# Performance work log

Measured on AMD Instinct MI355X. Metric: run time of the kernel, lower is better.

## Reference

```python
import jax, jax.numpy as jnp
import numpy as np

SEQ, B, IN, H = 512, 256, 300, 256

def setup_inputs() -> dict:
    key = jax.random.key(0)
    ks = jax.random.split(key, 14)
    s = lambda *sh: 1.0 / np.sqrt(sh[0])
    inp = {
        'secuencia': jax.random.normal(ks[0], (SEQ, B, IN), jnp.float32),
        # RNN cell 1 (forward direction)
        'W1x': jax.random.normal(ks[1], (IN, H), jnp.float32) * s(IN),
        'W1h': jax.random.normal(ks[2], (H, H), jnp.float32) * s(H),
        'b1':  jax.random.normal(ks[3], (H,), jnp.float32) * 0.01,
        # RNN cell 2 (backward direction)
        'W2x': jax.random.normal(ks[4], (IN, H), jnp.float32) * s(IN),
        'W2h': jax.random.normal(ks[5], (H, H), jnp.float32) * s(H),
        'b2':  jax.random.normal(ks[6], (H,), jnp.float32) * 0.01,
        # MLP head (weights stored [in, out])
        'fc1_w': jax.random.normal(ks[7], (2 * H, 2 * H), jnp.float32) * s(2 * H),
        'fc1_b': jnp.zeros((2 * H,), jnp.float32),
        'fc2_w': jax.random.normal(ks[8], (2 * H, H), jnp.float32) * s(2 * H),
        'fc2_b': jnp.zeros((H,), jnp.float32),
        'fs_w':  jax.random.normal(ks[9], (H, 1), jnp.float32) * s(H),
        'fs_b':  jnp.zeros((1,), jnp.float32),
    }
    return inp

def _rnn_scan(seq, Wx, Wh, b):
    # seq: [S, B, IN] -> final hidden [B, H]; Elman cell h' = tanh(x Wx + h Wh + b)
    h0 = jnp.zeros((seq.shape[1], Wh.shape[0]), seq.dtype)
    def step(h, x):
        return jnp.tanh(x @ Wx + h @ Wh + b), None
    h_final, _ = jax.lax.scan(step, h0, seq)
    return h_final

def reference(secuencia, W1x, W1h, b1, W2x, W2h, b2,
              fc1_w, fc1_b, fc2_w, fc2_b, fs_w, fs_b):
    h1 = _rnn_scan(secuencia, W1x, W1h, b1)          # forward pass over time
    h2 = _rnn_scan(secuencia[::-1], W2x, W2h, b2)    # reversed pass over time
    h = jnp.concatenate([h1, h2], axis=1)            # [B, 2H]
    x = jax.nn.relu(h @ fc1_w + fc1_b)
    x = jax.nn.relu(x @ fc2_w + fc2_b)
    out = jnp.tanh(x @ fs_w + fs_b)                  # [B, 1]
    return out.squeeze()
```

## Files before the change

kernel.cpp:

```cpp
#include <hip/hip_runtime.h>

#define DI __device__ __forceinline__

typedef float f32x4 __attribute__((ext_vector_type(4)));
typedef float f4    __attribute__((ext_vector_type(4)));
typedef _Float16 h8 __attribute__((ext_vector_type(8)));
typedef _Float16 h4 __attribute__((ext_vector_type(4)));

#define SEQL 512
#define BATCH 256
#define INF 300
#define HID 256
#define N2 512
#define KP 320


DI float ftanh(float x) {
    float e = __builtin_amdgcn_exp2f(x * 2.8853900817779268f);
    return fmaf(-2.0f, __builtin_amdgcn_rcpf(e + 1.0f), 1.0f);
}

__global__ void prep_kernel(const float* __restrict__ W1x, const float* __restrict__ W2x,
                            const float* __restrict__ b1, const float* __restrict__ b2,
                            _Float16* __restrict__ WTs, float* __restrict__ bcat)
{
    int idx = blockIdx.x * 256 + threadIdx.x;
    if (idx < N2 * KP) {
        int j = idx / KP, z = idx - j * KP;
        int k = z ^ ((j & 7) << 3);
        float v = 0.f;
        if (k < INF) v = (j < HID) ? W1x[k * HID + j] : W2x[k * HID + (j - HID)];
        WTs[j * KP + z] = (_Float16)v;
    }
    if (idx < N2) bcat[idx] = (idx < HID) ? b1[idx] : b2[idx - HID];
}

__global__ __launch_bounds__(512, 2) void gemm_pre(
    const float* __restrict__ x, const _Float16* __restrict__ WTs,
    const float* __restrict__ bcat, _Float16* __restrict__ pre3)
{
    __shared__ _Float16 Ab[128 * 64];
    __shared__ _Float16 Bb[256 * 64];
    const int tid = threadIdx.x;
    const int w = tid >> 6, l = tid & 63;
    const int lj = l & 15, lg = l >> 4;
    const int bid = blockIdx.x;
    const int xcd = bid & 7;
    const int idx0 = bid >> 3;
    const int jn = idx0 & 1;
    const int bm = xcd * 128 + (idx0 >> 1);
    const size_t m0 = (size_t)bm * 128;
    const int j0b = jn * 256;
    const int wj = (w >> 1) * 64, wm2 = (w & 1) * 64;

    f32x4 acc[4][4];
#pragma unroll
    for (int a = 0; a < 4; ++a)
#pragma unroll
        for (int b = 0; b < 4; ++b) acc[a][b] = f32x4{0.f, 0.f, 0.f, 0.f};

    for (int s = 0; s < 5; ++s) {
        const int k0 = s * 64;
#pragma unroll
        for (int q = 0; q < 4; ++q) {
            int idx = q * 512 + tid;
            int jr = idx >> 3, sl = idx & 7;
            const _Float16* src = WTs + (size_t)(j0b + jr) * KP + k0 + sl * 8;
            _Float16* dst = &Bb[(q * 512 + w * 64) * 8];
            __builtin_amdgcn_global_load_lds(
                (const __attribute__((address_space(1))) void*)src,
                (__attribute__((address_space(3))) void*)dst, 16, 0, 0);
        }
#pragma unroll
        for (int c = 0; c < 4; ++c) {
            int f = c * 512 + tid;
            int mr = f >> 4, k4 = f & 15;
            f4 v;
            if (k0 + k4 * 4 + 3 < INF)
                v = *(const f4*)(x + (m0 + mr) * INF + k0 + k4 * 4);
            else
                v = f4{0.f, 0.f, 0.f, 0.f};
            unsigned bo = (unsigned)mr * 128 + (((unsigned)k4 * 8) ^ ((mr & 7) << 4));
            *(h4*)((char*)Ab + bo) = h4{(_Float16)v[0], (_Float16)v[1], (_Float16)v[2], (_Float16)v[3]};
        }
        __syncthreads();
#pragma unroll
        for (int kk = 0; kk < 2; ++kk) {
            h8 aw[4], bx[4];
#pragma unroll
            for (int jt = 0; jt < 4; ++jt) {
                int jr = wj + jt * 16 + lj;
                unsigned bo = (unsigned)jr * 128 + (((unsigned)(kk * 64 + lg * 16)) ^ ((jr & 7) << 4));
                aw[jt] = *(const h8*)((const char*)Bb + bo);
            }
#pragma unroll
            for (int mt = 0; mt < 4; ++mt) {
                int mr = wm2 + mt * 16 + lj;
                unsigned bo = (unsigned)mr * 128 + (((unsigned)(kk * 64 + lg * 16)) ^ ((mr & 7) << 4));
                bx[mt] = *(const h8*)((const char*)Ab + bo);
            }
#pragma unroll
            for (int jt = 0; jt < 4; ++jt)
#pragma unroll
                for (int mt = 0; mt < 4; ++mt)
                    acc[jt][mt] = __builtin_amdgcn_mfma_f32_16x16x32_f16(aw[jt], bx[mt], acc[jt][mt], 0, 0, 0);
        }
        __syncthreads();
    }
    f4 bias4[4];
#pragma unroll
    for (int jt = 0; jt < 4; ++jt)
        bias4[jt] = *(const f4*)(bcat + j0b + wj + jt * 16 + lg * 4);
    char* prc = (char*)pre3;
#pragma unroll
    for (int jt = 0; jt < 4; ++jt) {
        int slab = (j0b + wj + jt * 16) >> 4;
#pragma unroll
        for (int mt = 0; mt < 4; ++mt) {
            int M = (int)m0 + wm2 + mt * 16;
            size_t byte = (size_t)(M >> 8) * 262144 + (size_t)slab * 8192
                        + (size_t)((M & 255) + lj) * 32 + (size_t)lg * 8;
            h4 o;
#pragma unroll
            for (int i = 0; i < 4; ++i)
                o[i] = (_Float16)(acc[jt][mt][i] + bias4[jt][i]);
            *(h4*)(prc + byte) = o;
        }
    }
}

__global__ __launch_bounds__(512, 2) void rnn_scan(
    const float* __restrict__ W1h, const float* __restrict__ W2h,
    const _Float16* __restrict__ pre3, float* __restrict__ hcat)
{
    __shared__ char hbs[16384];
    char* hbc = hbs;
    const int tid = threadIdx.x;
    const int w = tid >> 6, l = tid & 63;
    const int lj = l & 15, lg = l >> 4;
    const int dir = blockIdx.x & 1;
    const int b0 = (int)(blockIdx.x >> 1) * 16;
    const float* Wh = dir ? W2h : W1h;
    const int j0 = w * 32;
    const int dirOff = dir ? HID : 0;

    h8 afrag[2][8];
#pragma unroll
    for (int jt = 0; jt < 2; ++jt) {
        int jc = j0 + jt * 16 + lj;
#pragma unroll
        for (int kk = 0; kk < 8; ++kk) {
            h8 t;
#pragma unroll
            for (int i = 0; i < 8; ++i) t[i] = (_Float16)Wh[(kk * 32 + lg * 8 + i) * HID + jc];
            afrag[jt][kk] = t;
        }
    }

    const unsigned rb = (unsigned)l * 16;
    const unsigned wb0 = (unsigned)w * 1024 + (unsigned)(lg >> 1) * 256
                       + (unsigned)lj * 16 + (unsigned)(lg & 1) * 8;

    ((h8*)hbs)[tid] = h8{0, 0, 0, 0, 0, 0, 0, 0};
    __syncthreads();

    const long long sb = dir ? -262144LL : 262144LL;
    const char* pp = (const char*)pre3 + (long long)(dir ? (SEQL - 1) : 0) * 262144
                   + (long long)dir * 131072
                   + (long long)w * 16384 + (long long)(b0 + lj) * 32 + lg * 8;
    h4 pA[2], pB[2];
#pragma unroll
    for (int jt = 0; jt < 2; ++jt) pA[jt] = *(const h4*)(pp + jt * 8192);
    pp += sb;
#pragma unroll
    for (int jt = 0; jt < 2; ++jt) pB[jt] = *(const h4*)(pp + jt * 8192);
    pp += sb;

#define RNN_STEP(RB, WB, P, DO_PF)                                                    \
    do {                                                                              \
        h8 bf[8];                                                                     \
        _Pragma("unroll")                                                             \
        for (int kk = 0; kk < 8; ++kk)                                                \
            bf[kk] = *(const h8*)(hbc + (RB) + kk * 1024 + rb);                       \
        f32x4 acc0, acc1;                                                             \
        _Pragma("unroll")                                                             \
        for (int i = 0; i < 4; ++i) { acc0[i] = (float)P[0][i]; acc1[i] = (float)P[1][i]; } \
        if (DO_PF) {                                                                  \
            P[0] = *(const h4*)(pp);                                                  \
            P[1] = *(const h4*)(pp + 8192);                                           \
            pp += sb;                                                                 \
        }                                                                             \
        _Pragma("unroll")                                                             \
        for (int kk = 0; kk < 8; ++kk)                                                \
            acc0 = __builtin_amdgcn_mfma_f32_16x16x32_f16(afrag[0][kk], bf[kk], acc0, 0, 0, 0); \
        h4 o0;                                                                        \
        _Pragma("unroll")                                                             \
        for (int i = 0; i < 4; ++i) o0[i] = (_Float16)ftanh(acc0[i]);                 \
        *(h4*)(hbc + (WB) + wb0) = o0;                                                \
        _Pragma("unroll")                                                             \
        for (int kk = 0; kk < 8; ++kk)                                                \
            acc1 = __builtin_amdgcn_mfma_f32_16x16x32_f16(afrag[1][kk], bf[kk], acc1, 0, 0, 0); \
        h4 o1;                                                                        \
        _Pragma("unroll")                                                             \
        for (int i = 0; i < 4; ++i) o1[i] = (_Float16)ftanh(acc1[i]);                 \
        *(h4*)(hbc + (WB) + wb0 + 512) = o1;                                          \
        __builtin_amdgcn_sched_barrier(0);                                            \
        asm volatile("s_waitcnt lgkmcnt(0)" ::: "memory");                            \
        __builtin_amdgcn_s_barrier();                                                 \
        __builtin_amdgcn_sched_barrier(0);                                            \
    } while (0)

    for (int tp = 0; tp < 255; ++tp) {
        RNN_STEP(0, 8192, pA, 1);
        RNN_STEP(8192, 0, pB, 1);
    }
    RNN_STEP(0, 8192, pA, 0);

    {
        f32x4 acc0, acc1;
#pragma unroll
        for (int i = 0; i < 4; ++i) { acc0[i] = (float)pB[0][i]; acc1[i] = (float)pB[1][i]; }
        h8 bf[8];
#pragma unroll
        for (int kk = 0; kk < 8; ++kk)
            bf[kk] = *(const h8*)(hbc + 8192 + kk * 1024 + rb);
#pragma unroll
        for (int kk = 0; kk < 8; ++kk) {
            acc0 = __builtin_amdgcn_mfma_f32_16x16x32_f16(afrag[0][kk], bf[kk], acc0, 0, 0, 0);
            acc1 = __builtin_amdgcn_mfma_f32_16x16x32_f16(afrag[1][kk], bf[kk], acc1, 0, 0, 0);
        }
        f4 v0, v1;
#pragma unroll
        for (int i = 0; i < 4; ++i) { v0[i] = ftanh(acc0[i]); v1[i] = ftanh(acc1[i]); }
        float* hc = hcat + (size_t)(b0 + lj) * N2 + dirOff + j0 + lg * 4;
        *(f4*)hc = v0;
        *(f4*)(hc + 16) = v1;
    }
#undef RNN_STEP
}

__global__ __launch_bounds__(256) void head_mlp(
    const float* __restrict__ hcat,
    const float* __restrict__ fc1w, const float* __restrict__ fc1b,
    const float* __restrict__ fc2w, const float* __restrict__ fc2b,
    const float* __restrict__ fsw, const float* __restrict__ fsb,
    float* __restrict__ out)
{
    __shared__ float hs[4 * 512];
    __shared__ float y1[4 * 512];
    __shared__ float y2[4 * 256];
    const int tid = threadIdx.x;
    const int b0 = blockIdx.x * 4;
    const int r = tid >> 6;
    const int lane = tid & 63;

#pragma unroll
    for (int c = 0; c < 2; ++c)
        ((f4*)hs)[c * 256 + tid] = ((const f4*)(hcat + (size_t)b0 * N2))[c * 256 + tid];
    __syncthreads();

    {
        const int j0 = lane * 8;
        f4 a0 = *(const f4*)(fc1b + j0);
        f4 a1 = *(const f4*)(fc1b + j0 + 4);
        for (int k = 0; k < 512; ++k) {
            float h = hs[r * 512 + k];
            f4 w0 = *(const f4*)(fc1w + (size_t)k * 512 + j0);
            f4 w1 = *(const f4*)(fc1w + (size_t)k * 512 + j0 + 4);
#pragma unroll
            for (int i = 0; i < 4; ++i) { a0[i] = fmaf(h, w0[i], a0[i]); a1[i] = fmaf(h, w1[i], a1[i]); }
        }
#pragma unroll
        for (int i = 0; i < 4; ++i) {
            y1[r * 512 + j0 + i]     = fmaxf(a0[i], 0.f);
            y1[r * 512 + j0 + 4 + i] = fmaxf(a1[i], 0.f);
        }
    }
    __syncthreads();

    {
        const int j2 = lane * 4;
        f4 a = *(const f4*)(fc2b + j2);
        for (int k = 0; k < 512; ++k) {
            float yv = y1[r * 512 + k];
            f4 w = *(const f4*)(fc2w + (size_t)k * 256 + j2);
#pragma unroll
            for (int i = 0; i < 4; ++i) a[i] = fmaf(yv, w[i], a[i]);
        }
#pragma unroll
        for (int i = 0; i < 4; ++i) y2[r * 256 + j2 + i] = fmaxf(a[i], 0.f);
    }
    __syncthreads();

    {
        float p = 0.f;
#pragma unroll
        for (int u = 0; u < 4; ++u)
            p = fmaf(y2[r * 256 + lane + u * 64], fsw[lane + u * 64], p);
#pragma unroll
        for (int off = 32; off > 0; off >>= 1) p += __shfl_down(p, off);
        if (lane == 0) out[b0 + r] = ftanh(p + fsb[0]);
    }
}

extern "C" void kernel_launch(void* const* d_in, const int* in_sizes, int n_in,
                              void* d_out, int out_size, void* d_ws, size_t ws_size,
                              hipStream_t stream)
{
    const float* x    = (const float*)d_in[0];
    const float* W1x  = (const float*)d_in[1];
    const float* W1h  = (const float*)d_in[2];
    const float* b1   = (const float*)d_in[3];
    const float* W2x  = (const float*)d_in[4];
    const float* W2h  = (const float*)d_in[5];
    const float* b2   = (const float*)d_in[6];
    const float* fc1w = (const float*)d_in[7];
    const float* fc1b = (const float*)d_in[8];
    const float* fc2w = (const float*)d_in[9];
    const float* fc2b = (const float*)d_in[10];
    const float* fsw  = (const float*)d_in[11];
    const float* fsb  = (const float*)d_in[12];

    char* ws = (char*)d_ws;
    size_t off = 0;
    _Float16* WTs = (_Float16*)(ws + off); off += (size_t)N2 * KP * sizeof(_Float16);
    float* bcat   = (float*)(ws + off);    off += (size_t)N2 * sizeof(float);
    float* hcat   = (float*)(ws + off);    off += (size_t)BATCH * N2 * sizeof(float);
    _Float16* pre3 = (_Float16*)(ws + off); off += (size_t)SEQL * BATCH * N2 * sizeof(_Float16);
    if (off > ws_size) return;

    prep_kernel<<<(N2 * KP + 255) / 256, 256, 0, stream>>>(W1x, W2x, b1, b2, WTs, bcat);
    gemm_pre<<<2048, 512, 0, stream>>>(x, WTs, bcat, pre3);
    rnn_scan<<<(BATCH / 16) * 2, 512, 0, stream>>>(W1h, W2h, pre3, hcat);
    head_mlp<<<64, 256, 0, stream>>>(hcat, fc1w, fc1b, fc2w, fc2b, fsw, fsb, (float*)d_out);
}
```

Baseline: 493.5 us.

## Pre-tile x-projection weights into MFMA fragment order and load A fragments directly

The prep kernel now packs the fp16 input-projection weights into fragment-major order: each 16-byte chunk is exactly what one lane reads for the 16x16x32 MFMA. Each gemm_pre thread loads x for its own fragment rows and writes LDS linearly. This removes the XOR-swizzle address math and makes LDS reads contiguous per lane. In exchange, the x global loads are less coalesced, since each lane reads 32 bytes from a different row with a 1200-byte stride, and the last K tile adds a scalar-load branch.

```diff
diff --git a/kernel.cpp b/kernel.cpp
--- a/kernel.cpp
+++ b/kernel.cpp
@@ -22,25 +22,33 @@
 
 __global__ void prep_kernel(const float* __restrict__ W1x, const float* __restrict__ W2x,
                             const float* __restrict__ b1, const float* __restrict__ b2,
-                            _Float16* __restrict__ WTs, float* __restrict__ bcat)
-{
-    int idx = blockIdx.x * 256 + threadIdx.x;
-    if (idx < N2 * KP) {
-        int j = idx / KP, z = idx - j * KP;
-        int k = z ^ ((j & 7) << 3);
-        float v = 0.f;
-        if (k < INF) v = (j < HID) ? W1x[k * HID + j] : W2x[k * HID + (j - HID)];
-        WTs[j * KP + z] = (_Float16)v;
-    }
-    if (idx < N2) bcat[idx] = (idx < HID) ? b1[idx] : b2[idx - HID];
+                            _Float16* __restrict__ WTs2, float* __restrict__ bcat)
+{
+    int c = blockIdx.x * 256 + threadIdx.x;
+    if (c < 2 * 5 * 2048) {
+        int jn = c / (5 * 2048);
+        int r = c - jn * (5 * 2048);
+        int s = r >> 11, cc = r & 2047;
+        int jt = cc >> 7, kk = (cc >> 6) & 1, lg = (cc >> 4) & 3, lj = cc & 15;
+        int j = jn * 256 + jt * 16 + lj;
+        int k0 = s * 64 + kk * 32 + lg * 8;
+        const float* W = (j < HID) ? W1x : W2x;
+        int jj = (j < HID) ? j : j - HID;
+        h8 v;
+#pragma unroll
+        for (int i = 0; i < 8; ++i)
+            v[i] = (k0 + i < INF) ? (_Float16)W[(k0 + i) * HID + jj] : (_Float16)0.f;
+        ((h8*)WTs2)[c] = v;
+    }
+    if (c < N2) bcat[c] = (c < HID) ? b1[c] : b2[c - HID];
 }
 
 __global__ __launch_bounds__(512, 2) void gemm_pre(
-    const float* __restrict__ x, const _Float16* __restrict__ WTs,
+    const float* __restrict__ x, const _Float16* __restrict__ WTs2,
     const float* __restrict__ bcat, _Float16* __restrict__ pre3)
 {
-    __shared__ _Float16 Ab[128 * 64];
-    __shared__ _Float16 Bb[256 * 64];
+    __shared__ _Float16 Ab[1024 * 8];
+    __shared__ _Float16 Bb[2048 * 8];
     const int tid = threadIdx.x;
     const int w = tid >> 6, l = tid & 63;
     const int lj = l & 15, lg = l >> 4;
@@ -59,46 +67,54 @@
 #pragma unroll
         for (int b = 0; b < 4; ++b) acc[a][b] = f32x4{0.f, 0.f, 0.f, 0.f};
 
+    const _Float16* Wsrc = WTs2 + (size_t)jn * (5 * 2048 * 8);
+    const int am = w * 16 + lj;
+    const float* xp = x + (m0 + am) * INF;
+    const int kAo = lg * 8;
+    char* AbC = (char*)Ab;
+    char* BbC = (char*)Bb;
+
     for (int s = 0; s < 5; ++s) {
-        const int k0 = s * 64;
 #pragma unroll
         for (int q = 0; q < 4; ++q) {
-            int idx = q * 512 + tid;
-            int jr = idx >> 3, sl = idx & 7;
-            const _Float16* src = WTs + (size_t)(j0b + jr) * KP + k0 + sl * 8;
+            const _Float16* src = Wsrc + ((size_t)s * 2048 + q * 512 + w * 64 + l) * 8;
             _Float16* dst = &Bb[(q * 512 + w * 64) * 8];
             __builtin_amdgcn_global_load_lds(
                 (const __attribute__((address_space(1))) void*)src,
                 (__attribute__((address_space(3))) void*)dst, 16, 0, 0);
         }
-#pragma unroll
-        for (int c = 0; c < 4; ++c) {
-            int f = c * 512 + tid;
-            int mr = f >> 4, k4 = f & 15;
-            f4 v;
-            if (k0 + k4 * 4 + 3 < INF)
-                v = *(const f4*)(x + (m0 + mr) * INF + k0 + k4 * 4);
-            else
-                v = f4{0.f, 0.f, 0.f, 0.f};
-            unsigned bo = (unsigned)mr * 128 + (((unsigned)k4 * 8) ^ ((mr & 7) << 4));
-            *(h4*)((char*)Ab + bo) = h4{(_Float16)v[0], (_Float16)v[1], (_Float16)v[2], (_Float16)v[3]};
+        {
+            const int kA = s * 64 + kAo;
+            f4 a0 = *(const f4*)(xp + kA);
+            f4 a1 = *(const f4*)(xp + kA + 4);
+            h8 v0;
+#pragma unroll
+            for (int i = 0; i < 4; ++i) { v0[i] = (_Float16)a0[i]; v0[4 + i] = (_Float16)a1[i]; }
+            h8 v1;
+            if (s < 4) {
+                f4 b0 = *(const f4*)(xp + kA + 32);
+                f4 b1 = *(const f4*)(xp + kA + 36);
+#pragma unroll
+                for (int i = 0; i < 4; ++i) { v1[i] = (_Float16)b0[i]; v1[4 + i] = (_Float16)b1[i]; }
+            } else {
+                const int k1 = kA + 32;
+#pragma unroll
+                for (int i = 0; i < 8; ++i)
+                    v1[i] = (k1 + i < INF) ? (_Float16)xp[k1 + i] : (_Float16)0.f;
+            }
+            *(h8*)(AbC + (w * 128 + l) * 16) = v0;
+            *(h8*)(AbC + (w * 128 + 64 + l) * 16) = v1;
         }
         __syncthreads();
 #pragma unroll
         for (int kk = 0; kk < 2; ++kk) {
             h8 aw[4], bx[4];
 #pragma unroll
-            for (int jt = 0; jt < 4; ++jt) {
-                int jr = wj + jt * 16 + lj;
-                unsigned bo = (unsigned)jr * 128 + (((unsigned)(kk * 64 + lg * 16)) ^ ((jr & 7) << 4));
-                aw[jt] = *(const h8*)((const char*)Bb + bo);
-            }
-#pragma unroll
-            for (int mt = 0; mt < 4; ++mt) {
-                int mr = wm2 + mt * 16 + lj;
-                unsigned bo = (unsigned)mr * 128 + (((unsigned)(kk * 64 + lg * 16)) ^ ((mr & 7) << 4));
-                bx[mt] = *(const h8*)((const char*)Ab + bo);
-            }
+            for (int jt = 0; jt < 4; ++jt)
+                aw[jt] = *(const h8*)(BbC + ((((wj >> 4) + jt) * 2 + kk) * 1024 + l * 16));
+#pragma unroll
+            for (int mt = 0; mt < 4; ++mt)
+                bx[mt] = *(const h8*)(AbC + ((((wm2 >> 4) + mt) * 2 + kk) * 1024 + l * 16));
 #pragma unroll
             for (int jt = 0; jt < 4; ++jt)
 #pragma unroll
@@ -323,14 +339,14 @@
 
     char* ws = (char*)d_ws;
     size_t off = 0;
-    _Float16* WTs = (_Float16*)(ws + off); off += (size_t)N2 * KP * sizeof(_Float16);
-    float* bcat   = (float*)(ws + off);    off += (size_t)N2 * sizeof(float);
-    float* hcat   = (float*)(ws + off);    off += (size_t)BATCH * N2 * sizeof(float);
+    _Float16* WTs2 = (_Float16*)(ws + off); off += (size_t)2 * 5 * 2048 * 8 * sizeof(_Float16);
+    float* bcat    = (float*)(ws + off);    off += (size_t)N2 * sizeof(float);
+    float* hcat    = (float*)(ws + off);    off += (size_t)BATCH * N2 * sizeof(float);
     _Float16* pre3 = (_Float16*)(ws + off); off += (size_t)SEQL * BATCH * N2 * sizeof(_Float16);
     if (off > ws_size) return;
 
-    prep_kernel<<<(N2 * KP + 255) / 256, 256, 0, stream>>>(W1x, W2x, b1, b2, WTs, bcat);
-    gemm_pre<<<2048, 512, 0, stream>>>(x, WTs, bcat, pre3);
+    prep_kernel<<<80, 256, 0, stream>>>(W1x, W2x, b1, b2, WTs2, bcat);
+    gemm_pre<<<2048, 512, 0, stream>>>(x, WTs2, bcat, pre3);
     rnn_scan<<<(BATCH / 16) * 2, 512, 0, stream>>>(W1h, W2h, pre3, hcat);
     head_mlp<<<64, 256, 0, stream>>>(hcat, fc1w, fc1b, fc2w, fc2b, fsw, fsb, (float*)d_out);
 }
```

After: 508.6 us. +3.1%, slower.

## Double-buffer LDS tiles in gemm_pre to overlap global loads with MFMA

Applied to the files above, without the earlier changes.

Gives the input-projection GEMM two LDS buffers for each operand. The next K-slice of weights (via global_load_lds) and of x (via registers) is fetched while MFMAs run on the current slice, which removes one barrier per iteration and hides load latency. LDS use per block doubles to about 96 KB, which may limit how many blocks fit per CU. The head kernel also gains an unused shared reduction plus an extra __syncthreads inside a per-row section, which looks like leftover debris.

```diff
diff --git a/kernel.cpp b/kernel.cpp
--- a/kernel.cpp
+++ b/kernel.cpp
@@ -39,8 +39,8 @@
     const float* __restrict__ x, const _Float16* __restrict__ WTs,
     const float* __restrict__ bcat, _Float16* __restrict__ pre3)
 {
-    __shared__ _Float16 Ab[128 * 64];
-    __shared__ _Float16 Bb[256 * 64];
+    __shared__ _Float16 AbD[2][128 * 64];
+    __shared__ _Float16 BbD[2][256 * 64];
     const int tid = threadIdx.x;
     const int w = tid >> 6, l = tid & 63;
     const int lj = l & 15, lg = l >> 4;
@@ -59,31 +59,76 @@
 #pragma unroll
         for (int b = 0; b < 4; ++b) acc[a][b] = f32x4{0.f, 0.f, 0.f, 0.f};
 
+    char* Acur = (char*)AbD[0];
+    char* Anxt = (char*)AbD[1];
+    char* Bcur = (char*)BbD[0];
+    char* Bnxt = (char*)BbD[1];
+
+    const int amr = w * 16;
+
+#define STAGE_W(K0, BDST)                                                             \
+    do {                                                                              \
+        _Pragma("unroll")                                                             \
+        for (int q = 0; q < 4; ++q) {                                                 \
+            int idx = q * 512 + tid;                                                  \
+            int jr = idx >> 3, sl = idx & 7;                                          \
+            const _Float16* src = WTs + (size_t)(j0b + jr) * KP + (K0) + sl * 8;      \
+            _Float16* dst = (_Float16*)(BDST) + (size_t)(q * 512 + w * 64) * 8;       \
+            __builtin_amdgcn_global_load_lds(                                         \
+                (const __attribute__((address_space(1))) void*)src,                   \
+                (__attribute__((address_space(3))) void*)dst, 16, 0, 0);              \
+        }                                                                             \
+    } while (0)
+
+#define LOAD_X(K0, XR)                                                                \
+    do {                                                                              \
+        _Pragma("unroll")                                                             \
+        for (int c = 0; c < 4; ++c) {                                                 \
+            int f = c * 512 + tid;                                                    \
+            int mr = f >> 4, k4 = f & 15;                                             \
+            if ((K0) + k4 * 4 + 3 < INF)                                              \
+                XR[c] = *(const f4*)(x + (m0 + mr) * INF + (K0) + k4 * 4);            \
+            else                                                                      \
+                XR[c] = f4{0.f, 0.f, 0.f, 0.f};                                       \
+        }                                                                             \
+    } while (0)
+
+#define WRITE_X(XR, ADST)                                                             \
+    do {                                                                              \
+        _Pragma("unroll")                                                             \
+        for (int c = 0; c < 4; ++c) {                                                 \
+            int f = c * 512 + tid;                                                    \
+            int mr = f >> 4, k4 = f & 15;                                             \
+            unsigned bo = (unsigned)mr * 128 + (((unsigned)k4 * 8) ^ ((mr & 7) << 4)); \
+            *(h4*)((ADST) + bo) = h4{(_Float16)XR[c][0], (_Float16)XR[c][1],          \
+                                     (_Float16)XR[c][2], (_Float16)XR[c][3]};         \
+        }                                                                             \
+    } while (0)
+
+#define GBARRIER()                                                                    \
+    do {                                                                              \
+        __builtin_amdgcn_sched_barrier(0);                                            \
+        asm volatile("s_waitcnt vmcnt(0) lgkmcnt(0)" ::: "memory");                   \
+        __builtin_amdgcn_s_barrier();                                                 \
+        __builtin_amdgcn_sched_barrier(0);                                            \
+    } while (0)
+
+    {
+        f4 xr[4];
+        STAGE_W(0, Bcur);
+        LOAD_X(0, xr);
+        asm volatile("s_waitcnt vmcnt(0)" ::: "memory");
+        WRITE_X(xr, Acur);
+        GBARRIER();
+    }
+
     for (int s = 0; s < 5; ++s) {
-        const int k0 = s * 64;
-#pragma unroll
-        for (int q = 0; q < 4; ++q) {
-            int idx = q * 512 + tid;
-            int jr = idx >> 3, sl = idx & 7;
-            const _Float16* src = WTs + (size_t)(j0b + jr) * KP + k0 + sl * 8;
-            _Float16* dst = &Bb[(q * 512 + w * 64) * 8];
-            __builtin_amdgcn_global_load_lds(
-                (const __attribute__((address_space(1))) void*)src,
-                (__attribute__((address_space(3))) void*)dst, 16, 0, 0);
-        }
-#pragma unroll
-        for (int c = 0; c < 4; ++c) {
-            int f = c * 512 + tid;
-            int mr = f >> 4, k4 = f & 15;
-            f4 v;
-            if (k0 + k4 * 4 + 3 < INF)
-                v = *(const f4*)(x + (m0 + mr) * INF + k0 + k4 * 4);
-            else
-                v = f4{0.f, 0.f, 0.f, 0.f};
-            unsigned bo = (unsigned)mr * 128 + (((unsigned)k4 * 8) ^ ((mr & 7) << 4));
-            *(h4*)((char*)Ab + bo) = h4{(_Float16)v[0], (_Float16)v[1], (_Float16)v[2], (_Float16)v[3]};
-        }
-        __syncthreads();
+        f4 xr[4];
+        if (s < 4) {
+            const int k0n = (s + 1) * 64;
+            STAGE_W(k0n, Bnxt);
+            LOAD_X(k0n, xr);
+        }
 #pragma unroll
         for (int kk = 0; kk < 2; ++kk) {
             h8 aw[4], bx[4];
@@ -91,13 +136,13 @@
             for (int jt = 0; jt < 4; ++jt) {
                 int jr = wj + jt * 16 + lj;
                 unsigned bo = (unsigned)jr * 128 + (((unsigned)(kk * 64 + lg * 16)) ^ ((jr & 7) << 4));
-                aw[jt] = *(const h8*)((const char*)Bb + bo);
+                aw[jt] = *(const h8*)(Bcur + bo);
             }
 #pragma unroll
             for (int mt = 0; mt < 4; ++mt) {
                 int mr = wm2 + mt * 16 + lj;
                 unsigned bo = (unsigned)mr * 128 + (((unsigned)(kk * 64 + lg * 16)) ^ ((mr & 7) << 4));
-                bx[mt] = *(const h8*)((const char*)Ab + bo);
+                bx[mt] = *(const h8*)(Acur + bo);
             }
 #pragma unroll
             for (int jt = 0; jt < 4; ++jt)
@@ -105,8 +150,19 @@
                 for (int mt = 0; mt < 4; ++mt)
                     acc[jt][mt] = __builtin_amdgcn_mfma_f32_16x16x32_f16(aw[jt], bx[mt], acc[jt][mt], 0, 0, 0);
         }
-        __syncthreads();
-    }
+        if (s < 4) {
+            asm volatile("s_waitcnt vmcnt(0)" ::: "memory");
+            WRITE_X(xr, Anxt);
+        }
+        GBARRIER();
+        char* t0 = Acur; Acur = Anxt; Anxt = t0;
+        char* t1 = Bcur; Bcur = Bnxt; Bnxt = t1;
+    }
+#undef STAGE_W
+#undef LOAD_X
+#undef WRITE_X
+#undef GBARRIER
+
     f4 bias4[4];
 #pragma unroll
     for (int jt = 0; jt < 4; ++jt)
@@ -127,6 +183,7 @@
             *(h4*)(prc + byte) = o;
         }
     }
+    (void)amr;
 }
 
 __global__ __launch_bounds__(512, 2) void rnn_scan(
@@ -299,6 +356,12 @@
             p = fmaf(y2[r * 256 + lane + u * 64], fsw[lane + u * 64], p);
 #pragma unroll
         for (int off = 32; off > 0; off >>= 1) p += __shfl_down(p, off);
+        __shared__ float red[4];
+        if ((tid & 63) == 0) red[tid >> 6] = p;
+        __syncthreads();
+        if (tid == 0) {
+            float s = red[0] + red[1] + red[2] + red[3];
+        }
         if (lane == 0) out[b0 + r] = ftanh(p + fsb[0]);
     }
 }
@@ -323,9 +386,9 @@
 
     char* ws = (char*)d_ws;
     size_t off = 0;
-    _Float16* WTs = (_Float16*)(ws + off); off += (size_t)N2 * KP * sizeof(_Float16);
-    float* bcat   = (float*)(ws + off);    off += (size_t)N2 * sizeof(float);
-    float* hcat   = (float*)(ws + off);    off += (size_t)BATCH * N2 * sizeof(float);
+    _Float16* WTs  = (_Float16*)(ws + off); off += (size_t)N2 * KP * sizeof(_Float16);
+    float* bcat    = (float*)(ws + off);    off += (size_t)N2 * sizeof(float);
+    float* hcat    = (float*)(ws + off);    off += (size_t)BATCH * N2 * sizeof(float);
     _Float16* pre3 = (_Float16*)(ws + off); off += (size_t)SEQL * BATCH * N2 * sizeof(_Float16);
     if (off > ws_size) return;
 
```

Measured after the change: 476.5 us. 1.04x faster.
